# Kernel optimization log

Hardware: AMD Instinct MI355X
Metric: run time of the kernel (lower is better)

The kernel has to match this reference:

```python
import jax, jax.numpy as jnp
import numpy as np

B, C, H, W = 4, 512, 64, 64
RED = 2
IC = C // RED  # inter_channels = 256


def _conv1x1(x, w, b):
    # mmcv ConvModule default: conv(+bias) then ReLU
    return jax.nn.relu(jnp.einsum('bchw,oc->bohw', x, w) + b[None, :, None, None])


def setup_inputs() -> dict:
    key = jax.random.key(0)
    ks = jax.random.split(key, 9)
    s_q = 0.02  # small init so exp(-dist) stays in a sane range
    return {
        'features': jax.random.normal(ks[0], (B, C, H, W), jnp.float32),
        'qw': jax.random.normal(ks[1], (IC, C), jnp.float32) * s_q,
        'qb': jnp.zeros((IC,), jnp.float32),
        'kw': jax.random.normal(ks[2], (IC, C), jnp.float32) * s_q,
        'kb': jnp.zeros((IC,), jnp.float32),
        'vw': jax.random.normal(ks[3], (C, C), jnp.float32) * s_q,
        'vb': jnp.zeros((C,), jnp.float32),
        'cw': jax.random.normal(ks[4], (IC, 2), jnp.float32) * s_q,
        'cb': jnp.zeros((IC,), jnp.float32),
    }


def reference(features, qw, qb, kw, kb, vw, vb, cw, cb):
    b, c, h, w = features.shape
    q = _conv1x1(features, qw, qb)   # [b, IC, h, w]
    k = _conv1x1(features, kw, kb)   # [b, IC, h, w]
    v = _conv1x1(features, vw, vb)   # [b, C,  h, w]

    # coordinate grid: channel 0 varies along w, channel 1 along h
    lin = jnp.linspace(-1.0, 1.0, h)
    A = jnp.broadcast_to(lin[None, :], (h, w))
    coord = jnp.broadcast_to(jnp.stack([A, A.T], axis=0)[None], (b, 2, h, w))
    cc = _conv1x1(coord, cw, cb)     # [b, IC, h, w]

    q = q + cc
    k = k + cc

    n = h * w
    Qf = q.reshape(b, -1, n).transpose(0, 2, 1)  # [b, n, IC]
    Kf = k.reshape(b, -1, n)                     # [b, IC, n]

    dots = jnp.einsum('bnc,bcm->bnm', Qf, Kf)    # [b, n, n]
    a_sq = jnp.sum(Qf * Qf, axis=-1)             # [b, n]
    b_sq = jnp.sum(Kf * Kf, axis=1)              # [b, n]
    D = a_sq[:, :, None] + b_sq[:, None, :] - 2.0 * dots
    S = jnp.exp(-D)
    S = S / (jnp.sum(S, axis=-1, keepdims=True) + 1e-14)

    Vf = v.reshape(b, c, n)                      # [b, C, n]
    out = jnp.einsum('bcn,bnm->bcm', Vf, S).reshape(b, c, h, w)
    return out + features
```

## Files before the change

kernel.cpp:

```cpp
#include <hip/hip_runtime.h>
#include <math.h>

#define BATCH 4
#define CH    512
#define ICH   256
#define NPIX  4096

typedef short short8 __attribute__((ext_vector_type(8)));
typedef float floatx4 __attribute__((ext_vector_type(4)));

#define BK   64
#define TS   136

static __device__ __forceinline__ unsigned short f2bf(float x) {
    union { float f; unsigned u; } v; v.f = x;
    unsigned r = (v.u + 0x7FFF + ((v.u >> 16) & 1)) >> 16;
    return (unsigned short)r;
}
static __device__ __forceinline__ float bf2f(unsigned short u) {
    union { unsigned u; float f; } v; v.u = ((unsigned)u) << 16; return v.f;
}
static __device__ __forceinline__ unsigned pack_bf(unsigned ue, unsigned uo) {
    return ((ue + 0x8000u) >> 16) | ((uo + 0x8000u) & 0xFFFF0000u);
}

static __device__ __forceinline__ void gld16(const unsigned short* g, unsigned short* l) {
    __builtin_amdgcn_global_load_lds(
        (const __attribute__((address_space(1))) unsigned int*)g,
        (__attribute__((address_space(3))) unsigned int*)l,
        16, 0, 0);
}

#define STAGE_TILE(L, M, row0, RS, k0)                                        \
    {                                                                         \
        int r_  = (it*32) + wid*8 + (lane >> 3);                              \
        int c_  = (lane & 7) ^ ((lane >> 3) & 7);                             \
        gld16(&M[(size_t)((row0) + r_)*(RS) + (k0) + c_*8],                   \
              &L[(it*32 + wid*8)*64]);                                        \
    }

#define FRAG(L, row, ks) \
    (*(const short8*)&L[(row)*64 + (((((ks)<<2) + quad) ^ (lo & 7)) << 3)])

__global__ __launch_bounds__(256)
void prep_w(const float* __restrict__ qw, const float* __restrict__ kw,
            const float* __restrict__ vw, unsigned short* __restrict__ Wb)
{
    int i = (blockIdx.x*256 + threadIdx.x) * 4;
    const float* src;
    int off;
    if (i < 256*512)            { src = qw; off = i; }
    else if (i < 512*512)       { src = kw; off = i - 256*512; }
    else                        { src = vw; off = i - 512*512; }
    float4 f = *(const float4*)&src[off];
    unsigned short pk[4] = { f2bf(f.x), f2bf(f.y), f2bf(f.z), f2bf(f.w) };
    *(uint2*)&Wb[i] = *(uint2*)pk;
}

__global__ __launch_bounds__(256)
void prep_ft(const float* __restrict__ feat, unsigned short* __restrict__ Ft)
{
    __shared__ unsigned short S[64][65];
    const int t = threadIdx.x;
    const int n0 = blockIdx.x * 64, c0 = blockIdx.y * 64, b = blockIdx.z;

    #pragma unroll
    for (int rep = 0; rep < 4; rep++) {
        int cl = rep*16 + (t >> 4), col4 = (t & 15) * 4;
        float4 f = *(const float4*)&feat[((size_t)b*CH + c0 + cl)*NPIX + n0 + col4];
        S[cl][col4 + 0] = f2bf(f.x);
        S[cl][col4 + 1] = f2bf(f.y);
        S[cl][col4 + 2] = f2bf(f.z);
        S[cl][col4 + 3] = f2bf(f.w);
    }
    __syncthreads();
    #pragma unroll
    for (int rep = 0; rep < 4; rep++) {
        int nn = rep*16 + (t >> 4), cq = t & 15;
        unsigned short h4[4];
        #pragma unroll
        for (int j = 0; j < 4; j++) h4[j] = S[cq*4 + j][nn];
        *(uint2*)&Ft[((size_t)b*NPIX + n0 + nn)*CH + c0 + cq*4] = *(uint2*)h4;
    }
}

__global__ __launch_bounds__(256)
void conv_mfma(const unsigned short* __restrict__ Ft,
               const unsigned short* __restrict__ Wb,
               const float* __restrict__ qb, const float* __restrict__ kb,
               const float* __restrict__ vb,
               const float* __restrict__ cw, const float* __restrict__ cb,
               unsigned short* __restrict__ Qt, unsigned short* __restrict__ Kt,
               unsigned short* __restrict__ Vt)
{
    __shared__ unsigned short SH[128*TS];
    unsigned short* L0 = SH;
    unsigned short* L2 = SH + 128*64;

    const int tid = threadIdx.x;
    const int wid = tid >> 6, lane = tid & 63, quad = lane >> 4, lo = lane & 15;
    const int n0 = blockIdx.x * 128;
    const int yb = blockIdx.y;
    const int bz = blockIdx.z;
    const int o_base = yb * 128;
    const int waveA = (wid >> 1) * 64, waveB = (wid & 1) * 64;
    const int is_v = (yb >= 4);
    const size_t fb = (size_t)bz*NPIX;

    floatx4 acc[4][4] = {};

    for (int k0 = 0; k0 < CH; k0 += BK) {
        #pragma unroll
        for (int it = 0; it < 4; it++) {
            STAGE_TILE(L0, Ft, fb + n0, CH, k0);
            STAGE_TILE(L2, Wb, o_base,  CH, k0);
        }
        __syncthreads();
        if (!is_v) {
            #pragma unroll
            for (int ks = 0; ks < 2; ks++) {
                short8 af[4], bw[4];
                #pragma unroll
                for (int i = 0; i < 4; i++) af[i] = FRAG(L0, waveA + i*16 + lo, ks);
                #pragma unroll
                for (int j = 0; j < 4; j++) bw[j] = FRAG(L2, waveB + j*16 + lo, ks);
                #pragma unroll
                for (int i = 0; i < 4; i++)
                    #pragma unroll
                    for (int j = 0; j < 4; j++)
                        acc[i][j] = __builtin_amdgcn_mfma_f32_16x16x32_bf16(af[i], bw[j], acc[i][j], 0, 0, 0);
            }
        } else {
            #pragma unroll
            for (int ks = 0; ks < 2; ks++) {
                short8 aw[4], bf[4];
                #pragma unroll
                for (int i = 0; i < 4; i++) aw[i] = FRAG(L2, waveA + i*16 + lo, ks);
                #pragma unroll
                for (int j = 0; j < 4; j++) bf[j] = FRAG(L0, waveB + j*16 + lo, ks);
                #pragma unroll
                for (int i = 0; i < 4; i++)
                    #pragma unroll
                    for (int j = 0; j < 4; j++)
                        acc[i][j] = __builtin_amdgcn_mfma_f32_16x16x32_bf16(aw[i], bf[j], acc[i][j], 0, 0, 0);
            }
        }
        __syncthreads();
    }

    const float step = 2.0f / 63.0f;
    if (!is_v) {
        const float* bp = (yb < 2) ? qb : kb;
        const int icg0 = (yb & 1) * 128;
        #pragma unroll
        for (int ib = 0; ib < 4; ib++) {
            int colL = waveB + ib*16 + lo;
            int ic = icg0 + colL;
            float bias = bp[ic];
            float cw0 = cw[ic*2+0], cw1 = cw[ic*2+1], cbv = cb[ic];
            #pragma unroll
            for (int ia = 0; ia < 4; ia++) {
                int rowL = waveA + ia*16 + quad*4;
                #pragma unroll
                for (int r = 0; r < 4; r++) {
                    int n = n0 + rowL + r;
                    float cx = -1.f + (n & 63)*step;
                    float cy = -1.f + (n >> 6)*step;
                    float v = fmaxf(acc[ia][ib][r] + bias, 0.f)
                            + fmaxf(cw0*cx + cw1*cy + cbv, 0.f);
                    unsigned u = __float_as_uint(v);
                    unsigned p = __shfl_xor(u, 1, 64);
                    if ((lo & 1) == 0)
                        *(unsigned*)&SH[(rowL + r)*TS + colL] = pack_bf(u, p);
                }
            }
        }
    } else {
        const int c_blk0 = (yb - 4) * 128;
        #pragma unroll
        for (int ia = 0; ia < 4; ia++) {
            int rowL = waveA + ia*16 + quad*4;
            #pragma unroll
            for (int r = 0; r < 4; r++) {
                float bias = vb[c_blk0 + rowL + r];
                #pragma unroll
                for (int ib = 0; ib < 4; ib++) {
                    int colL = waveB + ib*16 + lo;
                    float v = fmaxf(acc[ia][ib][r] + bias, 0.f);
                    unsigned u = __float_as_uint(v);
                    unsigned p = __shfl_xor(u, 1, 64);
                    if ((lo & 1) == 0)
                        *(unsigned*)&SH[(rowL + r)*TS + colL] = pack_bf(u, p);
                }
            }
        }
    }
    __syncthreads();

    unsigned short* dstp;
    int row0, rs, col0;
    if (!is_v) { dstp = ((yb < 2) ? Qt : Kt) + (size_t)bz*NPIX*ICH;
                 row0 = n0; rs = ICH; col0 = (yb & 1) * 128; }
    else       { dstp = Vt + (size_t)bz*CH*NPIX;
                 row0 = (yb - 4) * 128; rs = NPIX; col0 = n0; }
    #pragma unroll
    for (int it = 0; it < 8; it++) {
        int f = it*256 + tid;
        int row = f >> 4, col = (f & 15) * 8;
        uint4 v = *(const uint4*)&SH[row*TS + col];
        *(uint4*)&dstp[(size_t)(row0 + row)*rs + col0 + col] = v;
    }
}

__global__ __launch_bounds__(256)
void sqb_kernel(const unsigned short* __restrict__ Qt,
                const unsigned short* __restrict__ Kt,
                float* __restrict__ asq, float* __restrict__ bsq)
{
    int n = blockIdx.x*256 + threadIdx.x;
    int b = blockIdx.y;
    const unsigned short* q = Qt + ((size_t)b*NPIX + n)*ICH;
    const unsigned short* k = Kt + ((size_t)b*NPIX + n)*ICH;
    float qs = 0.f, ks = 0.f;
    #pragma unroll 4
    for (int i = 0; i < ICH/8; i++) {
        uint4 v = *(const uint4*)&q[i*8];
        const unsigned short* s = (const unsigned short*)&v;
        #pragma unroll
        for (int j = 0; j < 8; j++) { float a = bf2f(s[j]); qs += a*a; }
        uint4 w = *(const uint4*)&k[i*8];
        const unsigned short* t = (const unsigned short*)&w;
        #pragma unroll
        for (int j = 0; j < 8; j++) { float a = bf2f(t[j]); ks += a*a; }
    }
    asq[b*NPIX + n] = qs;
    bsq[b*NPIX + n] = ks;
}

__global__ __launch_bounds__(256)
void dots_mfma(const unsigned short* __restrict__ Kt_,
               const unsigned short* __restrict__ Qt_,
               const float* __restrict__ asq_, const float* __restrict__ bsq_,
               unsigned short* __restrict__ St_, float* __restrict__ rsum_,
               int b0)
{
    __shared__ unsigned short SH[128*TS];
    unsigned short* Al = SH;
    unsigned short* Bl = SH + 128*64;

    const int tid = threadIdx.x;
    const int wid = tid >> 6, lane = tid & 63, quad = lane >> 4, lo = lane & 15;
    const int m0 = blockIdx.x * 128, n0 = blockIdx.y * 128;
    const int bz = blockIdx.z, gb = b0 + bz;
    const int waveM = (wid >> 1) * 64, waveN = (wid & 1) * 64;

    const unsigned short* Kt = Kt_ + (size_t)gb*NPIX*ICH;
    const unsigned short* Qt = Qt_ + (size_t)gb*NPIX*ICH;
    const float* asq = asq_ + (size_t)gb*NPIX;
    const float* bsq = bsq_ + (size_t)gb*NPIX;
    unsigned short* St = St_ + (size_t)bz*NPIX*NPIX;
    float* rsum = rsum_ + (size_t)gb*NPIX;

    floatx4 acc[4][4] = {};

    for (int k0 = 0; k0 < ICH; k0 += BK) {
        #pragma unroll
        for (int it = 0; it < 4; it++) {
            STAGE_TILE(Al, Kt, m0, ICH, k0);
            STAGE_TILE(Bl, Qt, n0, ICH, k0);
        }
        __syncthreads();
        #pragma unroll
        for (int ks = 0; ks < 2; ks++) {
            short8 a[4], bfr[4];
            #pragma unroll
            for (int im = 0; im < 4; im++) a[im]  = FRAG(Al, waveM + im*16 + lo, ks);
            #pragma unroll
            for (int in = 0; in < 4; in++) bfr[in] = FRAG(Bl, waveN + in*16 + lo, ks);
            #pragma unroll
            for (int im = 0; im < 4; im++)
                #pragma unroll
                for (int in = 0; in < 4; in++)
                    acc[im][in] = __builtin_amdgcn_mfma_f32_16x16x32_bf16(
                        a[im], bfr[in], acc[im][in], 0, 0, 0);
        }
        __syncthreads();
    }

    #pragma unroll
    for (int in = 0; in < 4; in++) {
        int nl = waveN + in*16 + lo;
        float aq = asq[n0 + nl];
        float colsum = 0.f;
        #pragma unroll
        for (int im = 0; im < 4; im++) {
            int mb = waveM + im*16 + quad*4;
            #pragma unroll
            for (int r = 0; r < 4; r++) {
                float d = aq + bsq[m0 + mb + r] - 2.f*acc[im][in][r];
                float s = __expf(-d);
                colsum += s;
                unsigned u = __float_as_uint(s);
                unsigned p = __shfl_xor(u, 1, 64);
                if ((lo & 1) == 0)
                    *(unsigned*)&SH[(mb + r)*TS + nl] = pack_bf(u, p);
            }
        }
        colsum += __shfl_xor(colsum, 16, 64);
        colsum += __shfl_xor(colsum, 32, 64);
        if (quad == 0) atomicAdd(&rsum[n0 + nl], colsum);
    }
    __syncthreads();

    #pragma unroll
    for (int it = 0; it < 8; it++) {
        int f = it*256 + tid;
        int row = f >> 4, col = (f & 15) * 8;
        uint4 v = *(const uint4*)&SH[row*TS + col];
        *(uint4*)&St[(size_t)(m0 + row)*NPIX + n0 + col] = v;
    }
}

__global__ __launch_bounds__(256)
void vscale_kernel(const unsigned short* __restrict__ Vt,
                   const float* __restrict__ rsum,
                   unsigned short* __restrict__ Vp, int b0)
{
    int gb = b0 + blockIdx.y;
    size_t base = (size_t)gb*CH*NPIX + ((size_t)blockIdx.x*256 + threadIdx.x) * 8;
    int n = (int)(base & (NPIX - 1));
    const float* rs = rsum + (size_t)gb*NPIX;
    uint4 v = *(const uint4*)&Vt[base];
    const unsigned short* s = (const unsigned short*)&v;
    unsigned short pk[8];
    #pragma unroll
    for (int i = 0; i < 8; i++)
        pk[i] = f2bf(bf2f(s[i]) / (rs[n + i] + 1e-14f));
    *(uint4*)&Vp[base] = *(uint4*)pk;
}

__global__ __launch_bounds__(256)
void pv_mfma(const unsigned short* __restrict__ Vp_,
             const unsigned short* __restrict__ St_,
             const float* __restrict__ feat_, float* __restrict__ out_,
             int b0)
{
    __shared__ unsigned short Al[128*64];
    __shared__ unsigned short Bl[128*64];
    const int tid = threadIdx.x;
    const int wid = tid >> 6, lane = tid & 63, quad = lane >> 4, lo = lane & 15;
    const int m0 = blockIdx.x * 128, c0 = blockIdx.y * 128;
    const int bz = blockIdx.z, gb = b0 + bz;
    const int waveA = (wid >> 1) * 64, waveB = (wid & 1) * 64;

    const unsigned short* Vp = Vp_ + (size_t)gb*CH*NPIX;
    const unsigned short* St = St_ + (size_t)bz*NPIX*NPIX;
    const float* feat = feat_ + (size_t)gb*CH*NPIX;
    float* out = out_ + (size_t)gb*CH*NPIX;

    floatx4 acc[4][4] = {};

    for (int k0 = 0; k0 < NPIX; k0 += BK) {
        #pragma unroll
        for (int it = 0; it < 4; it++) {
            STAGE_TILE(Al, Vp, c0, NPIX, k0);
            STAGE_TILE(Bl, St, m0, NPIX, k0);
        }
        __syncthreads();
        #pragma unroll
        for (int ks = 0; ks < 2; ks++) {
            short8 a[4], bfr[4];
            #pragma unroll
            for (int ia = 0; ia < 4; ia++) a[ia]  = FRAG(Al, waveA + ia*16 + lo, ks);
            #pragma unroll
            for (int ib = 0; ib < 4; ib++) bfr[ib] = FRAG(Bl, waveB + ib*16 + lo, ks);
            #pragma unroll
            for (int ia = 0; ia < 4; ia++)
                #pragma unroll
                for (int ib = 0; ib < 4; ib++)
                    acc[ia][ib] = __builtin_amdgcn_mfma_f32_16x16x32_bf16(
                        a[ia], bfr[ib], acc[ia][ib], 0, 0, 0);
        }
        __syncthreads();
    }

    #pragma unroll
    for (int ia = 0; ia < 4; ia++) {
        int cb = c0 + waveA + ia*16 + quad*4;
        #pragma unroll
        for (int r = 0; r < 4; r++) {
            size_t rowbase = (size_t)(cb + r)*NPIX;
            #pragma unroll
            for (int ib = 0; ib < 4; ib++) {
                int m = m0 + waveB + ib*16 + lo;
                out[rowbase + m] = acc[ia][ib][r] + feat[rowbase + m];
            }
        }
    }
}

extern "C" void kernel_launch(void* const* d_in, const int* in_sizes, int n_in,
                              void* d_out, int out_size, void* d_ws, size_t ws_size,
                              hipStream_t stream)
{
    const float* feat = (const float*)d_in[0];
    const float* qw   = (const float*)d_in[1];
    const float* qb   = (const float*)d_in[2];
    const float* kw   = (const float*)d_in[3];
    const float* kb   = (const float*)d_in[4];
    const float* vw   = (const float*)d_in[5];
    const float* vb   = (const float*)d_in[6];
    const float* cw   = (const float*)d_in[7];
    const float* cb   = (const float*)d_in[8];
    float* out = (float*)d_out;
    char* ws = (char*)d_ws;
    char* ws0 = ws;

    unsigned short* Ft  = (unsigned short*)ws;  ws += (size_t)BATCH*NPIX*CH*2;
    unsigned short* Wb  = (unsigned short*)ws;  ws += (size_t)1024*CH*2;
    unsigned short* Qt  = (unsigned short*)ws;  ws += (size_t)BATCH*NPIX*ICH*2;
    unsigned short* Kt  = (unsigned short*)ws;  ws += (size_t)BATCH*NPIX*ICH*2;
    unsigned short* Vt  = (unsigned short*)ws;  ws += (size_t)BATCH*CH*NPIX*2;
    unsigned short* Vp  = (unsigned short*)ws;  ws += (size_t)BATCH*CH*NPIX*2;
    float*         asq  = (float*)ws;           ws += (size_t)BATCH*NPIX*4;
    float*         bsq  = (float*)ws;           ws += (size_t)BATCH*NPIX*4;
    float*         rsum = (float*)ws;           ws += (size_t)BATCH*NPIX*4;
    unsigned short* St  = (unsigned short*)ws;

    const size_t st1 = (size_t)NPIX*NPIX*2;
    const size_t fixed = (size_t)(ws - ws0);
    const int nb = (ws_size >= fixed + (size_t)BATCH*st1) ? BATCH : 1;

    hipMemsetAsync(rsum, 0, (size_t)BATCH*NPIX*sizeof(float), stream);

    prep_w<<<dim3(512), 256, 0, stream>>>(qw, kw, vw, Wb);
    prep_ft<<<dim3(NPIX/64, CH/64, BATCH), 256, 0, stream>>>(feat, Ft);

    conv_mfma<<<dim3(NPIX/128, 8, BATCH), 256, 0, stream>>>(
        Ft, Wb, qb, kb, vb, cw, cb, Qt, Kt, Vt);

    sqb_kernel<<<dim3(NPIX/256, BATCH), 256, 0, stream>>>(Qt, Kt, asq, bsq);

    for (int b0 = 0; b0 < BATCH; b0 += nb) {
        dots_mfma<<<dim3(NPIX/128, NPIX/128, nb), 256, 0, stream>>>(
            Kt, Qt, asq, bsq, St, rsum, b0);
        vscale_kernel<<<dim3(CH*NPIX/(256*8), nb), 256, 0, stream>>>(
            Vt, rsum, Vp, b0);
        pv_mfma<<<dim3(NPIX/128, CH/128, nb), 256, 0, stream>>>(
            Vp, St, feat, out, b0);
    }
}
```

Measured before the change: 332.2 us.

## Triple-buffer PV GEMM with 256x128 tiles and 512-thread blocks

Rewrites the P·V MFMA kernel to use 512-thread blocks computing 128x256 output tiles. Global-to-LDS loads go into a three-stage ring of buffers, so the tile two steps ahead is fetched while the current one is computed. Loads are interleaved between two MFMA phases, with explicit vmcnt waits, raw barriers and setprio. The larger LDS footprint (about 144KB) and heavier register use may reduce occupancy.

After: 306.3 us. 7.8% less time.

```diff
diff --git a/kernel.cpp b/kernel.cpp
--- a/kernel.cpp
+++ b/kernel.cpp
@@ -37,6 +37,14 @@
         int c_  = (lane & 7) ^ ((lane >> 3) & 7);                             \
         gld16(&M[(size_t)((row0) + r_)*(RS) + (k0) + c_*8],                   \
               &L[(it*32 + wid*8)*64]);                                        \
+    }
+
+#define STG64(L, M, row0, RS, k0, u)                                          \
+    {                                                                         \
+        int r_  = (u)*64 + wid*8 + (lane >> 3);                               \
+        int c_  = (lane & 7) ^ ((lane >> 3) & 7);                             \
+        gld16(&M[(size_t)((row0) + r_)*(RS) + (k0) + c_*8],                   \
+              &L[((u)*64 + wid*8)*64]);                                       \
     }
 
 #define FRAG(L, row, ks) \
@@ -339,19 +347,22 @@
     *(uint4*)&Vp[base] = *(uint4*)pk;
 }
 
-__global__ __launch_bounds__(256)
+#define PVBUF 24576
+#define PVNT  (NPIX/BK)
+
+__global__ __launch_bounds__(512)
 void pv_mfma(const unsigned short* __restrict__ Vp_,
              const unsigned short* __restrict__ St_,
              const float* __restrict__ feat_, float* __restrict__ out_,
              int b0)
 {
-    __shared__ unsigned short Al[128*64];
-    __shared__ unsigned short Bl[128*64];
+    __shared__ unsigned short SH3[3*PVBUF];
     const int tid = threadIdx.x;
     const int wid = tid >> 6, lane = tid & 63, quad = lane >> 4, lo = lane & 15;
-    const int m0 = blockIdx.x * 128, c0 = blockIdx.y * 128;
+    const int wm = wid >> 2;
+    const int wn = wid & 3;
+    const int m0 = blockIdx.x * 256, c0 = blockIdx.y * 128;
     const int bz = blockIdx.z, gb = b0 + bz;
-    const int waveA = (wid >> 1) * 64, waveB = (wid & 1) * 64;
 
     const unsigned short* Vp = Vp_ + (size_t)gb*CH*NPIX;
     const unsigned short* St = St_ + (size_t)bz*NPIX*NPIX;
@@ -360,40 +371,97 @@
 
     floatx4 acc[4][4] = {};
 
-    for (int k0 = 0; k0 < NPIX; k0 += BK) {
-        #pragma unroll
-        for (int it = 0; it < 4; it++) {
-            STAGE_TILE(Al, Vp, c0, NPIX, k0);
-            STAGE_TILE(Bl, St, m0, NPIX, k0);
-        }
-        __syncthreads();
+    {
+        unsigned short* A0 = SH3;            unsigned short* B0 = SH3 + 128*64;
+        unsigned short* A1 = SH3 + PVBUF;    unsigned short* B1 = A1  + 128*64;
+        STG64(A0, Vp, c0, NPIX, 0, 0);  STG64(A0, Vp, c0, NPIX, 0, 1);
+        STG64(B0, St, m0, NPIX, 0, 0);  STG64(B0, St, m0, NPIX, 0, 1);
+        STG64(B0, St, m0, NPIX, 0, 2);  STG64(B0, St, m0, NPIX, 0, 3);
+        STG64(A1, Vp, c0, NPIX, BK, 0); STG64(A1, Vp, c0, NPIX, BK, 1);
+        STG64(B1, St, m0, NPIX, BK, 0); STG64(B1, St, m0, NPIX, BK, 1);
+        STG64(B1, St, m0, NPIX, BK, 2); STG64(B1, St, m0, NPIX, BK, 3);
+    }
+    asm volatile("s_waitcnt vmcnt(6)" ::: "memory");
+    __builtin_amdgcn_s_barrier();
+
+    int pc = 0, pn = 2;
+    for (int s = 0; s < PVNT; ++s) {
+        unsigned short* Ac = SH3 + pc*PVBUF;
+        unsigned short* Bc = Ac + 128*64;
+        unsigned short* An = SH3 + pn*PVBUF;
+        unsigned short* Bn = An + 128*64;
+        const int k2 = (s + 2) * BK;
+        const bool stg = (s < PVNT - 2);
+
+        short8 a0[2][4], b01[2][2];
         #pragma unroll
         for (int ks = 0; ks < 2; ks++) {
-            short8 a[4], bfr[4];
-            #pragma unroll
-            for (int ia = 0; ia < 4; ia++) a[ia]  = FRAG(Al, waveA + ia*16 + lo, ks);
-            #pragma unroll
-            for (int ib = 0; ib < 4; ib++) bfr[ib] = FRAG(Bl, waveB + ib*16 + lo, ks);
-            #pragma unroll
-            for (int ia = 0; ia < 4; ia++)
-                #pragma unroll
-                for (int ib = 0; ib < 4; ib++)
-                    acc[ia][ib] = __builtin_amdgcn_mfma_f32_16x16x32_bf16(
-                        a[ia], bfr[ib], acc[ia][ib], 0, 0, 0);
-        }
-        __syncthreads();
-    }
-
-    #pragma unroll
-    for (int ia = 0; ia < 4; ia++) {
-        int cb = c0 + waveA + ia*16 + quad*4;
+            #pragma unroll
+            for (int i = 0; i < 4; i++)
+                a0[ks][i] = FRAG(Ac, wm*64 + i*16 + lo, ks);
+            #pragma unroll
+            for (int j = 0; j < 2; j++)
+                b01[ks][j] = FRAG(Bc, wn*64 + j*16 + lo, ks);
+        }
+        if (stg) {
+            STG64(An, Vp, c0, NPIX, k2, 0);
+            STG64(An, Vp, c0, NPIX, k2, 1);
+            STG64(Bn, St, m0, NPIX, k2, 0);
+        }
+        __builtin_amdgcn_s_barrier();
+        __builtin_amdgcn_s_setprio(1);
+        #pragma unroll
+        for (int ks = 0; ks < 2; ks++)
+            #pragma unroll
+            for (int i = 0; i < 4; i++)
+                #pragma unroll
+                for (int j = 0; j < 2; j++)
+                    acc[i][j] = __builtin_amdgcn_mfma_f32_16x16x32_bf16(
+                        a0[ks][i], b01[ks][j], acc[i][j], 0, 0, 0);
+        __builtin_amdgcn_s_setprio(0);
+        __builtin_amdgcn_s_barrier();
+
+        short8 b23[2][2];
+        #pragma unroll
+        for (int ks = 0; ks < 2; ks++)
+            #pragma unroll
+            for (int j = 0; j < 2; j++)
+                b23[ks][j] = FRAG(Bc, wn*64 + (j+2)*16 + lo, ks);
+        if (stg) {
+            STG64(Bn, St, m0, NPIX, k2, 1);
+            STG64(Bn, St, m0, NPIX, k2, 2);
+            STG64(Bn, St, m0, NPIX, k2, 3);
+        }
+        __builtin_amdgcn_s_barrier();
+        __builtin_amdgcn_s_setprio(1);
+        #pragma unroll
+        for (int ks = 0; ks < 2; ks++)
+            #pragma unroll
+            for (int i = 0; i < 4; i++)
+                #pragma unroll
+                for (int j = 0; j < 2; j++)
+                    acc[i][j+2] = __builtin_amdgcn_mfma_f32_16x16x32_bf16(
+                        a0[ks][i], b23[ks][j], acc[i][j+2], 0, 0, 0);
+        __builtin_amdgcn_s_setprio(0);
+
+        if (s < PVNT - 2)       asm volatile("s_waitcnt vmcnt(6)" ::: "memory");
+        else if (s == PVNT - 2) asm volatile("s_waitcnt vmcnt(0)" ::: "memory");
+        __builtin_amdgcn_s_barrier();
+
+        pc = (pc == 2) ? 0 : pc + 1;
+        pn = (pn == 2) ? 0 : pn + 1;
+    }
+
+    #pragma unroll
+    for (int i = 0; i < 4; i++) {
+        int cr = c0 + wm*64 + i*16 + quad*4;
         #pragma unroll
         for (int r = 0; r < 4; r++) {
-            size_t rowbase = (size_t)(cb + r)*NPIX;
-            #pragma unroll
-            for (int ib = 0; ib < 4; ib++) {
-                int m = m0 + waveB + ib*16 + lo;
-                out[rowbase + m] = acc[ia][ib][r] + feat[rowbase + m];
+            size_t rowbase = (size_t)(cr + r)*NPIX;
+            #pragma unroll
+            for (int j = 0; j < 4; j++) {
+                int m = m0 + wn*64 + j*16 + lo;
+                out[rowbase + m] = acc[i][j][r] + feat[rowbase + m];
             }
         }
     }
@@ -446,7 +514,7 @@
             Kt, Qt, asq, bsq, St, rsum, b0);
         vscale_kernel<<<dim3(CH*NPIX/(256*8), nb), 256, 0, stream>>>(
             Vt, rsum, Vp, b0);
-        pv_mfma<<<dim3(NPIX/128, CH/128, nb), 256, 0, stream>>>(
+        pv_mfma<<<dim3(NPIX/256, CH/128, nb), 512, 0, stream>>>(
             Vp, St, feat, out, b0);
     }
 }
```
